# Kernel tuning notes

Measured on AMD Instinct MI355X. Metric: run time of the kernel, lower is better.

The kernel has to match this reference:

```python
import jax, jax.numpy as jnp
import numpy as np

HOP = 5
NP_, NA_ = 100000, 100000


def spmm(src, dst, w, h, n_dst):
    # sparse.mm(A1, h): gather source rows, weight, scatter-add to destinations
    return jax.ops.segment_sum(h[src] * w[:, None], dst, num_segments=n_dst)


def sem_att(out, W1, b1, w2):
    # out: [N, R, D] stacked per-relation embeddings (HAN semantic attention)
    s = jnp.einsum('nrh,h->nr', jnp.tanh(jnp.einsum('nrd,dh->nrh', out, W1) + b1), w2)
    beta = jax.nn.softmax(jnp.mean(s, axis=0))  # [R]
    return jnp.einsum('nrd,r->nd', out, beta)


def setup_inputs() -> dict:
    key = jax.random.key(0)
    ks = jax.random.split(key, 32)
    E = 1600000
    inp = {
        'x_paper': jax.random.normal(ks[0], (NP_, 256), jnp.float32),
        'x_author': jax.random.normal(ks[1], (NA_, 128), jnp.float32),
        'fc1p_W': jax.random.normal(ks[2], (256, 128), jnp.float32) * 0.05,
        'fc1p_b': jnp.zeros((128,), jnp.float32),
        'fc1a_W': jax.random.normal(ks[3], (128, 128), jnp.float32) * 0.05,
        'fc1a_b': jnp.zeros((128,), jnp.float32),
        'fc2_W': jax.random.normal(ks[4], (128, 64), jnp.float32) * 0.05,
        'fc2_b': jnp.zeros((64,), jnp.float32),
        'semW1': jax.random.normal(ks[5], (HOP, 2, 128, 128), jnp.float32) * 0.05,
        'semb1': jnp.zeros((HOP, 2, 128), jnp.float32),
        'semw2': jax.random.normal(ks[6], (HOP, 2, 128), jnp.float32) * 0.05,
        'd_pp': jax.random.uniform(ks[7], (NP_, 1), jnp.float32),
        'd_pa': jax.random.uniform(ks[8], (NP_, 1), jnp.float32),
        'd_ap': jax.random.uniform(ks[9], (NA_, 1), jnp.float32),
        'd_aa': jax.random.uniform(ks[10], (NA_, 1), jnp.float32),
        'w_pp': jax.random.uniform(ks[11], (E,), jnp.float32) * 0.0625,
        'w_pa': jax.random.uniform(ks[12], (E,), jnp.float32) * 0.0625,
        'w_ap': jax.random.uniform(ks[13], (E,), jnp.float32) * 0.0625,
        'w_aa': jax.random.uniform(ks[14], (E,), jnp.float32) * 0.0625,
        'src_pp': jax.random.randint(ks[15], (E,), 0, NP_, jnp.int32),
        'dst_pp': jax.random.randint(ks[16], (E,), 0, NP_, jnp.int32),
        'src_pa': jax.random.randint(ks[17], (E,), 0, NA_, jnp.int32),
        'dst_pa': jax.random.randint(ks[18], (E,), 0, NP_, jnp.int32),
        'src_ap': jax.random.randint(ks[19], (E,), 0, NP_, jnp.int32),
        'dst_ap': jax.random.randint(ks[20], (E,), 0, NA_, jnp.int32),
        'src_aa': jax.random.randint(ks[21], (E,), 0, NA_, jnp.int32),
        'dst_aa': jax.random.randint(ks[22], (E,), 0, NA_, jnp.int32),
    }
    return inp


def reference(x_paper, x_author, fc1p_W, fc1p_b, fc1a_W, fc1a_b, fc2_W, fc2_b,
              semW1, semb1, semw2, d_pp, d_pa, d_ap, d_aa,
              w_pp, w_pa, w_ap, w_aa,
              src_pp, dst_pp, src_pa, dst_pa, src_ap, dst_ap, src_aa, dst_aa):
    # type-specific input projection (dropout is identity in eval mode)
    x_p = jax.nn.relu(x_paper @ fc1p_W + fc1p_b)   # [NP, H]
    x_a = jax.nn.relu(x_author @ fc1a_W + fc1a_b)  # [NA, H]
    h_p, h_a = x_p, x_a
    for i in range(HOP):
        # paper node type: relations (paper<-paper, paper<-author); uses old h_p, h_a
        hp_rel = jnp.stack([
            spmm(src_pp, dst_pp, w_pp, h_p, NP_) + d_pp * x_p,
            spmm(src_pa, dst_pa, w_pa, h_a, NP_) + d_pa * x_p,
        ], axis=1)  # [NP, 2, H]
        h_p = sem_att(hp_rel, semW1[i, 0], semb1[i, 0], semw2[i, 0])
        # author node type: relations (author<-paper, author<-author); uses updated h_p (sequential, as in torch)
        ha_rel = jnp.stack([
            spmm(src_ap, dst_ap, w_ap, h_p, NA_) + d_ap * x_a,
            spmm(src_aa, dst_aa, w_aa, h_a, NA_) + d_aa * x_a,
        ], axis=1)  # [NA, 2, H]
        h_a = sem_att(ha_rel, semW1[i, 1], semb1[i, 1], semw2[i, 1])
    return h_p @ fc2_W + fc2_b  # target_node_type = 'paper'
```

## Files before the change

### kernel.cpp

```cpp
#include <hip/hip_runtime.h>


typedef __attribute__((ext_vector_type(8))) short bf16x8;
typedef __attribute__((ext_vector_type(4))) float f32x4;
typedef __attribute__((ext_vector_type(4))) unsigned u32x4;
typedef __attribute__((ext_vector_type(2))) int i32x2;
typedef unsigned short ushort_t;

__device__ inline unsigned short f2bf(float f) {
  union { float f; unsigned u; } x; x.f = f;
  unsigned r = x.u + 0x7fff + ((x.u >> 16) & 1);
  return (unsigned short)(r >> 16);
}
__device__ inline float bf2f(unsigned short u) {
  union { unsigned u; float f; } x; x.u = (unsigned)u << 16; return x.f;
}
__device__ inline float i2f(int i) {
  union { int i; float f; } x; x.i = i; return x.f;
}
__device__ inline int f2i(float f) {
  union { float f; int i; } x; x.f = f; return x.i;
}
__device__ inline void unpack8(u32x4 u, float* f) {
  union { unsigned u; float f; } c;
  c.u = u.x << 16;          f[0] = c.f;
  c.u = u.x & 0xffff0000u;  f[1] = c.f;
  c.u = u.y << 16;          f[2] = c.f;
  c.u = u.y & 0xffff0000u;  f[3] = c.f;
  c.u = u.z << 16;          f[4] = c.f;
  c.u = u.z & 0xffff0000u;  f[5] = c.f;
  c.u = u.w << 16;          f[6] = c.f;
  c.u = u.w & 0xffff0000u;  f[7] = c.f;
}
__device__ inline u32x4 pack8(const float* f) {
  u32x4 u;
  u.x = (unsigned)f2bf(f[0]) | ((unsigned)f2bf(f[1]) << 16);
  u.y = (unsigned)f2bf(f[2]) | ((unsigned)f2bf(f[3]) << 16);
  u.z = (unsigned)f2bf(f[4]) | ((unsigned)f2bf(f[5]) << 16);
  u.w = (unsigned)f2bf(f[6]) | ((unsigned)f2bf(f[7]) << 16);
  return u;
}

__global__ void zero_kernel(float* __restrict__ p, int n) {
  int i = blockIdx.x * blockDim.x + threadIdx.x;
  if (i < n) p[i] = 0.f;
}

__global__ void hist_kernel(const int* __restrict__ dst, int E, int* __restrict__ cnt) {
  int i = blockIdx.x * blockDim.x + threadIdx.x;
  if (i < E) atomicAdd(&cnt[dst[i]], 1);
}

__global__ void scan4_kernel(const int* __restrict__ cnt, int* __restrict__ rp,
                             int* __restrict__ cur, int Np, int Na) {
  __shared__ int wsum[16];
  __shared__ int carry_s;
  int r = blockIdx.x;
  int N = (r < 2) ? Np : Na;
  size_t coff  = (r==0)?0 : (r==1)? (size_t)Np : (r==2)? (size_t)2*Np : (size_t)2*Np+Na;
  size_t rpoff = (r==0)?0 : (r==1)? (size_t)(Np+1) : (r==2)? (size_t)2*(Np+1) : (size_t)2*(Np+1)+(Na+1);
  const int* c = cnt + coff;
  int* rpp = rp + rpoff;
  int* cpp = cur + coff;
  int tid = threadIdx.x;
  int lane = tid & 63, wv = tid >> 6;
  if (tid == 0) carry_s = 0;
  for (int base = 0; base < N; base += 1024) {
    int i = base + tid;
    int v = (i < N) ? c[i] : 0;
    int s = v;
#pragma unroll
    for (int off = 1; off < 64; off <<= 1) {
      int t = __shfl_up(s, off);
      if (lane >= off) s += t;
    }
    if (lane == 63) wsum[wv] = s;
    __syncthreads();
    if (wv == 0 && lane < 16) {
      int p = wsum[lane];
      int q = p;
#pragma unroll
      for (int off = 1; off < 16; off <<= 1) {
        int t = __shfl_up(q, off);
        if (lane >= off) q += t;
      }
      wsum[lane] = q - p;
    }
    __syncthreads();
    int carry = carry_s;
    int wexcl = wsum[wv];
    int excl = carry + wexcl + (s - v);
    if (i < N) { rpp[i] = excl; cpp[i] = excl; }
    int mytotal = wexcl + s;
    __syncthreads();
    if (tid == 1023) carry_s = carry + mytotal;
  }
  __syncthreads();
  if (tid == 0) rpp[N] = carry_s;
}

__global__ void scatter_kernel(const int* __restrict__ src, const int* __restrict__ dst,
                               const float* __restrict__ w, int* __restrict__ cur,
                               i32x2* __restrict__ cw, int E) {
  int i = blockIdx.x * blockDim.x + threadIdx.x;
  if (i < E) {
    int p = atomicAdd(&cur[dst[i]], 1);
    i32x2 v; v.x = src[i]; v.y = f2i(w[i]);
    cw[p] = v;
  }
}

template<int K, int KH>
__global__ __launch_bounds__(256) void fc1_mfma_kernel(
    const float* __restrict__ x, const float* __restrict__ W,
    const float* __restrict__ b, ushort_t* __restrict__ o1, ushort_t* __restrict__ o2,
    int N) {
  constexpr int TPB = 4 / KH;
  __shared__ float cstage[4][16][128];
  int tid = threadIdx.x;
  int lane = tid & 63, wid = tid >> 6;
  int tile = (KH == 2) ? (wid >> 1) : wid;
  int khalf = (KH == 2) ? (wid & 1) : 0;
  int r = lane & 15, kg = lane >> 4;
  bf16x8 bfr[8][4];
#pragma unroll
  for (int jt = 0; jt < 8; jt++) {
    int j = jt * 16 + r;
#pragma unroll
    for (int kt = 0; kt < 4; kt++) {
      int k0 = khalf * 128 + kt * 32 + kg * 8;
      bf16x8 v;
#pragma unroll
      for (int t = 0; t < 8; t++) v[t] = (short)f2bf(W[(size_t)(k0 + t) * 128 + j]);
      bfr[jt][kt] = v;
    }
  }
  float bb[8];
  {
    int j0 = (tid & 15) * 8;
#pragma unroll
    for (int t = 0; t < 8; t++) bb[t] = b[j0 + t];
  }
  int ntiles = (N + 15) >> 4;
  int tstride = gridDim.x * TPB;
  for (int tb = blockIdx.x * TPB; tb < ntiles; tb += tstride) {
    int mytile = tb + tile;
    int nodeA = mytile * 16 + r;
    if (nodeA >= N) nodeA = 0;
    const float* xrow = x + (size_t)nodeA * K + khalf * 128;
    bf16x8 afr[4];
#pragma unroll
    for (int kt = 0; kt < 4; kt++) {
      const f32x4* p = (const f32x4*)(xrow + kt * 32 + kg * 8);
      f32x4 lo = __builtin_nontemporal_load(p);
      f32x4 hi = __builtin_nontemporal_load(p + 1);
      bf16x8 v;
      v[0] = (short)f2bf(lo.x); v[1] = (short)f2bf(lo.y);
      v[2] = (short)f2bf(lo.z); v[3] = (short)f2bf(lo.w);
      v[4] = (short)f2bf(hi.x); v[5] = (short)f2bf(hi.y);
      v[6] = (short)f2bf(hi.z); v[7] = (short)f2bf(hi.w);
      afr[kt] = v;
    }
    f32x4 acc[8];
#pragma unroll
    for (int jt = 0; jt < 8; jt++) acc[jt] = (f32x4){0.f, 0.f, 0.f, 0.f};
#pragma unroll
    for (int jt = 0; jt < 8; jt++)
#pragma unroll
      for (int kt = 0; kt < 4; kt++)
        acc[jt] = __builtin_amdgcn_mfma_f32_16x16x32_bf16(afr[kt], bfr[jt][kt], acc[jt], 0, 0, 0);
#pragma unroll
    for (int jt = 0; jt < 8; jt++)
#pragma unroll
      for (int reg = 0; reg < 4; reg++)
        cstage[wid][kg * 4 + reg][jt * 16 + r] = acc[jt][reg];
    __syncthreads();
    int node = tid >> 4, j0 = (tid & 15) * 8;
#pragma unroll
    for (int it = 0; it < TPB; it++) {
      int n = (tb + it) * 16 + node;
      float f[8];
#pragma unroll
      for (int t = 0; t < 8; t++) {
        float v = cstage[it * KH][node][j0 + t];
        if (KH == 2) v += cstage[it * 2 + 1][node][j0 + t];
        f[t] = fmaxf(v + bb[t], 0.f);
      }
      if (n < N) {
        u32x4 pk = pack8(f);
        *(u32x4*)(o1 + (size_t)n * 128 + j0) = pk;
        *(u32x4*)(o2 + (size_t)n * 128 + j0) = pk;
      }
    }
    __syncthreads();
  }
}

__global__ __launch_bounds__(256) void spmm2_kernel(
    const ushort_t* __restrict__ xself,
    const float* __restrict__ d0, const float* __restrict__ d1,
    const ushort_t* __restrict__ h0, const ushort_t* __restrict__ h1,
    const int* __restrict__ rp0, const i32x2* __restrict__ cw0,
    const int* __restrict__ rp1, const i32x2* __restrict__ cw1,
    ushort_t* __restrict__ rel, int N) {
  int tid = threadIdx.x;
  int lane = tid & 63, wid = tid >> 6;
  int fg = lane & 15;
  int eslot = lane >> 4;
  int n = blockIdx.x * 4 + wid;
  if (n >= N) return;
  float xf[8];
  unpack8(*(const u32x4*)(xself + (size_t)n * 128 + fg * 8), xf);
#pragma unroll
  for (int srel = 0; srel < 2; srel++) {
    const float sd = srel ? d1[n] : d0[n];
    const int* rp = srel ? rp1 : rp0;
    const i32x2* cw = srel ? cw1 : cw0;
    const ushort_t* h = srel ? h1 : h0;
    float acc[8];
#pragma unroll
    for (int t = 0; t < 8; t++) acc[t] = 0.f;
    int beg = rp[n], end = rp[n + 1];
    for (int cb = beg; cb < end; cb += 64) {
      int m = end - cb; if (m > 64) m = 64;
      int creg = 0, wbits = 0;
      if (lane < m) {
        i32x2 p = __builtin_nontemporal_load(&cw[cb + lane]);
        creg = p.x; wbits = p.y;
      }
      int i = 0;
      for (; i + 16 <= m; i += 16) {
        int e0 = i + eslot, e1 = i + 4 + eslot, e2 = i + 8 + eslot, e3 = i + 12 + eslot;
        int   c0 = __shfl(creg, e0), c1 = __shfl(creg, e1);
        int   c2 = __shfl(creg, e2), c3 = __shfl(creg, e3);
        float v0 = i2f(__shfl(wbits, e0)), v1 = i2f(__shfl(wbits, e1));
        float v2 = i2f(__shfl(wbits, e2)), v3 = i2f(__shfl(wbits, e3));
        u32x4 g0 = *(const u32x4*)(h + (size_t)c0 * 128 + fg * 8);
        u32x4 g1 = *(const u32x4*)(h + (size_t)c1 * 128 + fg * 8);
        u32x4 g2 = *(const u32x4*)(h + (size_t)c2 * 128 + fg * 8);
        u32x4 g3 = *(const u32x4*)(h + (size_t)c3 * 128 + fg * 8);
        float hf[8];
        unpack8(g0, hf);
#pragma unroll
        for (int t = 0; t < 8; t++) acc[t] = fmaf(v0, hf[t], acc[t]);
        unpack8(g1, hf);
#pragma unroll
        for (int t = 0; t < 8; t++) acc[t] = fmaf(v1, hf[t], acc[t]);
        unpack8(g2, hf);
#pragma unroll
        for (int t = 0; t < 8; t++) acc[t] = fmaf(v2, hf[t], acc[t]);
        unpack8(g3, hf);
#pragma unroll
        for (int t = 0; t < 8; t++) acc[t] = fmaf(v3, hf[t], acc[t]);
      }
      for (; i < m; i += 4) {
        int e = i + eslot;
        int   c = __shfl(creg, e & 63);
        float v = i2f(__shfl(wbits, e & 63));
        if (e < m) {
          u32x4 g = *(const u32x4*)(h + (size_t)c * 128 + fg * 8);
          float hf[8];
          unpack8(g, hf);
#pragma unroll
          for (int t = 0; t < 8; t++) acc[t] = fmaf(v, hf[t], acc[t]);
        }
      }
    }
#pragma unroll
    for (int t = 0; t < 8; t++) {
      acc[t] += __shfl_xor(acc[t], 16);
      acc[t] += __shfl_xor(acc[t], 32);
    }
    if (eslot == 0) {
#pragma unroll
      for (int t = 0; t < 8; t++) acc[t] = fmaf(sd, xf[t], acc[t]);
      __builtin_nontemporal_store(pack8(acc),
          (u32x4*)(rel + (size_t)n * 256 + srel * 128 + fg * 8));
    }
  }
}

__global__ __launch_bounds__(256) void score_mfma_kernel(
    const ushort_t* __restrict__ rel,
    const float* __restrict__ W1,
    const float* __restrict__ b1, const float* __restrict__ w2,
    float* __restrict__ s_out, int N, int nwaves) {
  int tid = threadIdx.x;
  int lane = tid & 63;
  int gw = blockIdx.x * 4 + (tid >> 6);
  int r = lane & 15;
  int kg = lane >> 4;
  bf16x8 bfr[8][4];
#pragma unroll
  for (int jt = 0; jt < 8; jt++) {
    int j = jt * 16 + r;
#pragma unroll
    for (int kt = 0; kt < 4; kt++) {
      int k0 = kt * 32 + kg * 8;
      bf16x8 v;
#pragma unroll
      for (int t = 0; t < 8; t++) v[t] = (short)f2bf(W1[(size_t)(k0 + t) * 128 + j]);
      bfr[jt][kt] = v;
    }
  }
  float b1v[8], w2v[8];
#pragma unroll
  for (int jt = 0; jt < 8; jt++) { b1v[jt] = b1[jt * 16 + r]; w2v[jt] = w2[jt * 16 + r]; }
  float s0 = 0.f, s1 = 0.f;
  int ntiles = (N + 15) >> 4;
  for (int tile = gw; tile < ntiles; tile += nwaves) {
    int n0 = tile * 16;
    int nodeA = n0 + r;
    size_t base = (size_t)((nodeA < N) ? nodeA : 0) * 256;
#pragma unroll
    for (int sub = 0; sub < 2; sub++) {
      bf16x8 afr[4];
#pragma unroll
      for (int kt = 0; kt < 4; kt++)
        afr[kt] = __builtin_nontemporal_load(
            (const bf16x8*)(rel + base + sub * 128 + kt * 32 + kg * 8));
      f32x4 acc[8];
#pragma unroll
      for (int jt = 0; jt < 8; jt++) acc[jt] = (f32x4){0.f, 0.f, 0.f, 0.f};
#pragma unroll
      for (int jt = 0; jt < 8; jt++)
#pragma unroll
        for (int kt = 0; kt < 4; kt++)
          acc[jt] = __builtin_amdgcn_mfma_f32_16x16x32_bf16(afr[kt], bfr[jt][kt], acc[jt], 0, 0, 0);
      float sacc = 0.f;
#pragma unroll
      for (int jt = 0; jt < 8; jt++) {
#pragma unroll
        for (int reg = 0; reg < 4; reg++) {
          int nm = n0 + kg * 4 + reg;
          if (nm < N) sacc += w2v[jt] * tanhf(acc[jt][reg] + b1v[jt]);
        }
      }
      if (sub == 0) s0 += sacc; else s1 += sacc;
    }
  }
#pragma unroll
  for (int m = 32; m >= 1; m >>= 1) { s0 += __shfl_xor(s0, m); s1 += __shfl_xor(s1, m); }
  if (lane == 0) { atomicAdd(&s_out[0], s0); atomicAdd(&s_out[1], s1); }
}

__global__ void combine_kernel(const ushort_t* __restrict__ rel, const float* __restrict__ s,
                               ushort_t* __restrict__ h, int N, float invN) {
  int i = blockIdx.x * blockDim.x + threadIdx.x;
  if (i >= N * 16) return;
  float m0 = s[0] * invN, m1 = s[1] * invN;
  float mx = fmaxf(m0, m1);
  float e0 = expf(m0 - mx), e1 = expf(m1 - mx);
  float inv = 1.f / (e0 + e1);
  float be0 = e0 * inv, be1 = e1 * inv;
  int n = i >> 4, q = i & 15;
  float f0[8], f1[8], o[8];
  unpack8(__builtin_nontemporal_load((const u32x4*)(rel + (size_t)n * 256 + q * 8)), f0);
  unpack8(__builtin_nontemporal_load((const u32x4*)(rel + (size_t)n * 256 + 128 + q * 8)), f1);
#pragma unroll
  for (int t = 0; t < 8; t++) o[t] = be0 * f0[t] + be1 * f1[t];
  *(u32x4*)(h + (size_t)n * 128 + q * 8) = pack8(o);
}

__global__ __launch_bounds__(256) void fc2_mfma_kernel(
    const ushort_t* __restrict__ h,
    const float* __restrict__ W,
    const float* __restrict__ b,
    float* __restrict__ out, int N, int nwaves) {
  int tid = threadIdx.x;
  int lane = tid & 63;
  int gw = blockIdx.x * 4 + (tid >> 6);
  int r = lane & 15, kg = lane >> 4;
  bf16x8 bfr[4][4];
#pragma unroll
  for (int jt = 0; jt < 4; jt++) {
    int j = jt * 16 + r;
#pragma unroll
    for (int kt = 0; kt < 4; kt++) {
      int k0 = kt * 32 + kg * 8;
      bf16x8 v;
#pragma unroll
      for (int t = 0; t < 8; t++) v[t] = (short)f2bf(W[(size_t)(k0 + t) * 64 + j]);
      bfr[jt][kt] = v;
    }
  }
  float bv[4];
#pragma unroll
  for (int jt = 0; jt < 4; jt++) bv[jt] = b[jt * 16 + r];
  int ntiles = (N + 15) >> 4;
  for (int tile = gw; tile < ntiles; tile += nwaves) {
    int n0 = tile * 16;
    int nodeA = n0 + r;
    const ushort_t* hrow = h + (size_t)((nodeA < N) ? nodeA : 0) * 128;
    bf16x8 afr[4];
#pragma unroll
    for (int kt = 0; kt < 4; kt++)
      afr[kt] = *(const bf16x8*)(hrow + kt * 32 + kg * 8);
    f32x4 acc[4];
#pragma unroll
    for (int jt = 0; jt < 4; jt++) acc[jt] = (f32x4){0.f, 0.f, 0.f, 0.f};
#pragma unroll
    for (int jt = 0; jt < 4; jt++)
#pragma unroll
      for (int kt = 0; kt < 4; kt++)
        acc[jt] = __builtin_amdgcn_mfma_f32_16x16x32_bf16(afr[kt], bfr[jt][kt], acc[jt], 0, 0, 0);
#pragma unroll
    for (int jt = 0; jt < 4; jt++)
#pragma unroll
      for (int reg = 0; reg < 4; reg++) {
        int n = n0 + kg * 4 + reg;
        if (n < N) out[(size_t)n * 64 + jt * 16 + r] = acc[jt][reg] + bv[jt];
      }
  }
}

extern "C" void kernel_launch(void* const* d_in, const int* in_sizes, int n_in,
                              void* d_out, int out_size, void* d_ws, size_t ws_size,
                              hipStream_t stream) {
  const float* x_paper  = (const float*)d_in[0];
  const float* x_author = (const float*)d_in[1];
  const float* fc1p_W = (const float*)d_in[2];
  const float* fc1p_b = (const float*)d_in[3];
  const float* fc1a_W = (const float*)d_in[4];
  const float* fc1a_b = (const float*)d_in[5];
  const float* fc2_W  = (const float*)d_in[6];
  const float* fc2_b  = (const float*)d_in[7];
  const float* semW1  = (const float*)d_in[8];
  const float* semb1  = (const float*)d_in[9];
  const float* semw2  = (const float*)d_in[10];
  const float* d_pp = (const float*)d_in[11];
  const float* d_pa = (const float*)d_in[12];
  const float* d_ap = (const float*)d_in[13];
  const float* d_aa = (const float*)d_in[14];
  const float* w_pp = (const float*)d_in[15];
  const float* w_pa = (const float*)d_in[16];
  const float* w_ap = (const float*)d_in[17];
  const float* w_aa = (const float*)d_in[18];
  const int* src_pp = (const int*)d_in[19];
  const int* dst_pp = (const int*)d_in[20];
  const int* src_pa = (const int*)d_in[21];
  const int* dst_pa = (const int*)d_in[22];
  const int* src_ap = (const int*)d_in[23];
  const int* dst_ap = (const int*)d_in[24];
  const int* src_aa = (const int*)d_in[25];
  const int* dst_aa = (const int*)d_in[26];

  const int Np = in_sizes[11];
  const int Na = in_sizes[13];
  const int E[4] = { in_sizes[15], in_sizes[16], in_sizes[17], in_sizes[18] };
  const int Nmax = (Np > Na) ? Np : Na;

  char* base = (char*)d_ws;
  size_t off = 0;
  ushort_t* xp = (ushort_t*)(base + off); off += (size_t)Np * 128 * 2;
  ushort_t* xa = (ushort_t*)(base + off); off += (size_t)Na * 128 * 2;
  ushort_t* hp = (ushort_t*)(base + off); off += (size_t)Np * 128 * 2;
  ushort_t* ha = (ushort_t*)(base + off); off += (size_t)Na * 128 * 2;
  ushort_t* rel = (ushort_t*)(base + off); off += (size_t)Nmax * 256 * 2;
  float* ssum = (float*)(base + off); off += 32 * 4;
  int* cnt  = (int*)(base + off); off += (size_t)(2 * Np + 2 * Na) * 4;
  int* rpB  = (int*)(base + off); off += (size_t)(2 * (Np + 1) + 2 * (Na + 1)) * 4;
  int* curB = (int*)(base + off); off += (size_t)(2 * Np + 2 * Na) * 4;
  size_t Esum = (size_t)E[0] + E[1] + E[2] + E[3];
  off = (off + 15) & ~(size_t)15;
  i32x2* cwB = (i32x2*)(base + off); off += Esum * 8;
  (void)ws_size; (void)n_in; (void)out_size;

  int* cnt_r[4] = { cnt, cnt + Np, cnt + (size_t)2 * Np, cnt + (size_t)2 * Np + Na };
  int* rp_r[4]  = { rpB, rpB + (Np + 1), rpB + (size_t)2 * (Np + 1),
                    rpB + (size_t)2 * (Np + 1) + (Na + 1) };
  int* cur_r[4] = { curB, curB + Np, curB + (size_t)2 * Np, curB + (size_t)2 * Np + Na };
  size_t eoff[4] = { 0, (size_t)E[0], (size_t)E[0] + E[1], (size_t)E[0] + E[1] + E[2] };
  i32x2* cw_r[4];
  for (int r = 0; r < 4; r++) cw_r[r] = cwB + eoff[r];

  const int* srcs[4]    = { src_pp, src_pa, src_ap, src_aa };
  const int* dsts[4]    = { dst_pp, dst_pa, dst_ap, dst_aa };
  const float* wedge[4] = { w_pp, w_pa, w_ap, w_aa };

  int Z = 32 + 2 * Np + 2 * Na;
  zero_kernel<<<(Z + 255) / 256, 256, 0, stream>>>(ssum, Z);

  for (int r = 0; r < 4; r++)
    hist_kernel<<<(E[r] + 255) / 256, 256, 0, stream>>>(dsts[r], E[r], cnt_r[r]);
  scan4_kernel<<<4, 1024, 0, stream>>>(cnt, rpB, curB, Np, Na);
  for (int r = 0; r < 4; r++)
    scatter_kernel<<<(E[r] + 255) / 256, 256, 0, stream>>>(srcs[r], dsts[r], wedge[r],
                                                           cur_r[r], cw_r[r], E[r]);

  fc1_mfma_kernel<256, 2><<<256, 256, 0, stream>>>(x_paper, fc1p_W, fc1p_b, xp, hp, Np);
  fc1_mfma_kernel<128, 1><<<256, 256, 0, stream>>>(x_author, fc1a_W, fc1a_b, xa, ha, Na);

  const int SCORE_BLOCKS = 256;
  const int SCORE_WAVES = SCORE_BLOCKS * 4;

  for (int i = 0; i < 5; i++) {
    float* sp = ssum + (size_t)(i * 2 + 0) * 2;
    spmm2_kernel<<<(Np + 3) / 4, 256, 0, stream>>>(xp, d_pp, d_pa, hp, ha,
        rp_r[0], cw_r[0], rp_r[1], cw_r[1], rel, Np);
    score_mfma_kernel<<<SCORE_BLOCKS, 256, 0, stream>>>(rel,
        semW1 + (size_t)(i * 2 + 0) * 16384, semb1 + (size_t)(i * 2 + 0) * 128,
        semw2 + (size_t)(i * 2 + 0) * 128, sp, Np, SCORE_WAVES);
    combine_kernel<<<(Np * 16 + 255) / 256, 256, 0, stream>>>(rel, sp, hp, Np, 1.f / Np);

    float* sa = ssum + (size_t)(i * 2 + 1) * 2;
    spmm2_kernel<<<(Na + 3) / 4, 256, 0, stream>>>(xa, d_ap, d_aa, hp, ha,
        rp_r[2], cw_r[2], rp_r[3], cw_r[3], rel, Na);
    score_mfma_kernel<<<SCORE_BLOCKS, 256, 0, stream>>>(rel,
        semW1 + (size_t)(i * 2 + 1) * 16384, semb1 + (size_t)(i * 2 + 1) * 128,
        semw2 + (size_t)(i * 2 + 1) * 128, sa, Na, SCORE_WAVES);
    combine_kernel<<<(Na * 16 + 255) / 256, 256, 0, stream>>>(rel, sa, ha, Na, 1.f / Na);
  }

  fc2_mfma_kernel<<<256, 256, 0, stream>>>(hp, fc2_W, fc2_b, (float*)d_out, Np, 1024);
}
```

Before: 2.896 ms.

## Fuse CSR build launches with fc1 and skip unused final author hop

Merges the four histogram launches into one kernel and folds the fc1 projections and the four scatter launches into a single build kernel that dispatches on block index. It also skips the author update in the last hop, because the output only depends on paper embeddings. This removes launch overhead and a full spmm/score/combine pass over authors, at the cost of extra register and shared-memory pressure from the merged fc1/scatter kernel.

```diff
diff --git a/kernel.cpp b/kernel.cpp
--- a/kernel.cpp
+++ b/kernel.cpp
@@ -11,9 +11,6 @@
   union { float f; unsigned u; } x; x.f = f;
   unsigned r = x.u + 0x7fff + ((x.u >> 16) & 1);
   return (unsigned short)(r >> 16);
-}
-__device__ inline float bf2f(unsigned short u) {
-  union { unsigned u; float f; } x; x.u = (unsigned)u << 16; return x.f;
 }
 __device__ inline float i2f(int i) {
   union { int i; float f; } x; x.i = i; return x.f;
@@ -46,9 +43,24 @@
   if (i < n) p[i] = 0.f;
 }
 
-__global__ void hist_kernel(const int* __restrict__ dst, int E, int* __restrict__ cnt) {
-  int i = blockIdx.x * blockDim.x + threadIdx.x;
-  if (i < E) atomicAdd(&cnt[dst[i]], 1);
+struct Hist4Args {
+  const int* dst[4];
+  int* cnt[4];
+  int E[4];
+  int nb[4];
+};
+
+__global__ void hist4_kernel(Hist4Args a) {
+  int vb = blockIdx.x;
+#pragma unroll
+  for (int r = 0; r < 4; r++) {
+    if (vb < a.nb[r]) {
+      int i = vb * 256 + threadIdx.x;
+      if (i < a.E[r]) atomicAdd(&a.cnt[r][a.dst[r][i]], 1);
+      return;
+    }
+    vb -= a.nb[r];
+  }
 }
 
 __global__ void scan4_kernel(const int* __restrict__ cnt, int* __restrict__ rp,
@@ -99,24 +111,12 @@
   if (tid == 0) rpp[N] = carry_s;
 }
 
-__global__ void scatter_kernel(const int* __restrict__ src, const int* __restrict__ dst,
-                               const float* __restrict__ w, int* __restrict__ cur,
-                               i32x2* __restrict__ cw, int E) {
-  int i = blockIdx.x * blockDim.x + threadIdx.x;
-  if (i < E) {
-    int p = atomicAdd(&cur[dst[i]], 1);
-    i32x2 v; v.x = src[i]; v.y = f2i(w[i]);
-    cw[p] = v;
-  }
-}
-
 template<int K, int KH>
-__global__ __launch_bounds__(256) void fc1_mfma_kernel(
+__device__ void fc1_body(float (*cstage)[16][128],
     const float* __restrict__ x, const float* __restrict__ W,
     const float* __restrict__ b, ushort_t* __restrict__ o1, ushort_t* __restrict__ o2,
-    int N) {
+    int N, int bid, int nblocks) {
   constexpr int TPB = 4 / KH;
-  __shared__ float cstage[4][16][128];
   int tid = threadIdx.x;
   int lane = tid & 63, wid = tid >> 6;
   int tile = (KH == 2) ? (wid >> 1) : wid;
@@ -142,8 +142,8 @@
     for (int t = 0; t < 8; t++) bb[t] = b[j0 + t];
   }
   int ntiles = (N + 15) >> 4;
-  int tstride = gridDim.x * TPB;
-  for (int tb = blockIdx.x * TPB; tb < ntiles; tb += tstride) {
+  int tstride = nblocks * TPB;
+  for (int tb = bid * TPB; tb < ntiles; tb += tstride) {
     int mytile = tb + tile;
     int nodeA = mytile * 16 + r;
     if (nodeA >= N) nodeA = 0;
@@ -193,6 +193,51 @@
       }
     }
     __syncthreads();
+  }
+}
+
+__device__ void scatter_body(const int* __restrict__ src, const int* __restrict__ dst,
+                             const float* __restrict__ w, int* __restrict__ cur,
+                             i32x2* __restrict__ cw, int E, int bid) {
+  int i = bid * 256 + threadIdx.x;
+  if (i < E) {
+    int p = atomicAdd(&cur[dst[i]], 1);
+    i32x2 v; v.x = src[i]; v.y = f2i(w[i]);
+    cw[p] = v;
+  }
+}
+
+struct BuildArgs {
+  const float* fx[2]; const float* fW[2]; const float* fb[2];
+  ushort_t* fo1[2]; ushort_t* fo2[2];
+  int fN[2]; int fB[2];
+  const int* src[4]; const int* dst[4]; const float* w[4];
+  int* cur[4]; i32x2* cw[4];
+  int E[4]; int nb[4];
+};
+
+__global__ __launch_bounds__(256) void build_kernel(BuildArgs a) {
+  __shared__ float cstage[4][16][128];
+  int vb = blockIdx.x;
+  if (vb < a.fB[0]) {
+    fc1_body<256, 2>(cstage, a.fx[0], a.fW[0], a.fb[0], a.fo1[0], a.fo2[0],
+                     a.fN[0], vb, a.fB[0]);
+    return;
+  }
+  vb -= a.fB[0];
+  if (vb < a.fB[1]) {
+    fc1_body<128, 1>(cstage, a.fx[1], a.fW[1], a.fb[1], a.fo1[1], a.fo2[1],
+                     a.fN[1], vb, a.fB[1]);
+    return;
+  }
+  vb -= a.fB[1];
+#pragma unroll
+  for (int r = 0; r < 4; r++) {
+    if (vb < a.nb[r]) {
+      scatter_body(a.src[r], a.dst[r], a.w[r], a.cur[r], a.cw[r], a.E[r], vb);
+      return;
+    }
+    vb -= a.nb[r];
   }
 }
 
@@ -481,15 +526,32 @@
   int Z = 32 + 2 * Np + 2 * Na;
   zero_kernel<<<(Z + 255) / 256, 256, 0, stream>>>(ssum, Z);
 
-  for (int r = 0; r < 4; r++)
-    hist_kernel<<<(E[r] + 255) / 256, 256, 0, stream>>>(dsts[r], E[r], cnt_r[r]);
+  Hist4Args ha_args;
+  int hist_blocks = 0;
+  for (int r = 0; r < 4; r++) {
+    ha_args.dst[r] = dsts[r];
+    ha_args.cnt[r] = cnt_r[r];
+    ha_args.E[r] = E[r];
+    ha_args.nb[r] = (E[r] + 255) / 256;
+    hist_blocks += ha_args.nb[r];
+  }
+  hist4_kernel<<<hist_blocks, 256, 0, stream>>>(ha_args);
+
   scan4_kernel<<<4, 1024, 0, stream>>>(cnt, rpB, curB, Np, Na);
-  for (int r = 0; r < 4; r++)
-    scatter_kernel<<<(E[r] + 255) / 256, 256, 0, stream>>>(srcs[r], dsts[r], wedge[r],
-                                                           cur_r[r], cw_r[r], E[r]);
-
-  fc1_mfma_kernel<256, 2><<<256, 256, 0, stream>>>(x_paper, fc1p_W, fc1p_b, xp, hp, Np);
-  fc1_mfma_kernel<128, 1><<<256, 256, 0, stream>>>(x_author, fc1a_W, fc1a_b, xa, ha, Na);
+
+  BuildArgs ba;
+  ba.fx[0] = x_paper;  ba.fW[0] = fc1p_W; ba.fb[0] = fc1p_b;
+  ba.fo1[0] = xp; ba.fo2[0] = hp; ba.fN[0] = Np; ba.fB[0] = 256;
+  ba.fx[1] = x_author; ba.fW[1] = fc1a_W; ba.fb[1] = fc1a_b;
+  ba.fo1[1] = xa; ba.fo2[1] = ha; ba.fN[1] = Na; ba.fB[1] = 256;
+  int build_blocks = ba.fB[0] + ba.fB[1];
+  for (int r = 0; r < 4; r++) {
+    ba.src[r] = srcs[r]; ba.dst[r] = dsts[r]; ba.w[r] = wedge[r];
+    ba.cur[r] = cur_r[r]; ba.cw[r] = cw_r[r]; ba.E[r] = E[r];
+    ba.nb[r] = (E[r] + 255) / 256;
+    build_blocks += ba.nb[r];
+  }
+  build_kernel<<<build_blocks, 256, 0, stream>>>(ba);
 
   const int SCORE_BLOCKS = 256;
   const int SCORE_WAVES = SCORE_BLOCKS * 4;
@@ -503,13 +565,15 @@
         semw2 + (size_t)(i * 2 + 0) * 128, sp, Np, SCORE_WAVES);
     combine_kernel<<<(Np * 16 + 255) / 256, 256, 0, stream>>>(rel, sp, hp, Np, 1.f / Np);
 
-    float* sa = ssum + (size_t)(i * 2 + 1) * 2;
-    spmm2_kernel<<<(Na + 3) / 4, 256, 0, stream>>>(xa, d_ap, d_aa, hp, ha,
-        rp_r[2], cw_r[2], rp_r[3], cw_r[3], rel, Na);
-    score_mfma_kernel<<<SCORE_BLOCKS, 256, 0, stream>>>(rel,
-        semW1 + (size_t)(i * 2 + 1) * 16384, semb1 + (size_t)(i * 2 + 1) * 128,
-        semw2 + (size_t)(i * 2 + 1) * 128, sa, Na, SCORE_WAVES);
-    combine_kernel<<<(Na * 16 + 255) / 256, 256, 0, stream>>>(rel, sa, ha, Na, 1.f / Na);
+    if (i < 4) {
+      float* sa = ssum + (size_t)(i * 2 + 1) * 2;
+      spmm2_kernel<<<(Na + 3) / 4, 256, 0, stream>>>(xa, d_ap, d_aa, hp, ha,
+          rp_r[2], cw_r[2], rp_r[3], cw_r[3], rel, Na);
+      score_mfma_kernel<<<SCORE_BLOCKS, 256, 0, stream>>>(rel,
+          semW1 + (size_t)(i * 2 + 1) * 16384, semb1 + (size_t)(i * 2 + 1) * 128,
+          semw2 + (size_t)(i * 2 + 1) * 128, sa, Na, SCORE_WAVES);
+      combine_kernel<<<(Na * 16 + 255) / 256, 256, 0, stream>>>(rel, sa, ha, Na, 1.f / Na);
+    }
   }
 
   fc2_mfma_kernel<<<256, 256, 0, stream>>>(hp, fc2_W, fc2_b, (float*)d_out, Np, 1024);
```

New measurement: 2.508 ms. 1.15x faster.
